# Kernel optimization log

Hardware: AMD Instinct MI355X
Metric: run time of the kernel (lower is better)

Reference implementation:

```python
import jax, jax.numpy as jnp
import numpy as np

B, S, V, E, H, NL, DFF = 16, 16, 64, 64, 8, 4, 2048
L = S * V
DH = E // H
NUM_GRIDS = 100
POI_DIM = 8
OV_DIM = 8


def setup_inputs() -> dict:
    key = jax.random.key(0)
    ks = jax.random.split(key, 32)
    sc = 0.05
    inp = {}
    inp['features'] = jax.random.normal(ks[0], (B, S, V, 3), jnp.float32)
    inp['overlap_tag'] = jax.random.randint(ks[1], (B, S, V), 0, 3)
    inp['poi_id'] = jax.random.randint(ks[2], (B, S, V), 0, NUM_GRIDS + 1)
    # embedders
    inp['W_raw'] = jax.random.normal(ks[3], (3, E), jnp.float32) * sc
    inp['b_raw'] = jnp.zeros((E,), jnp.float32)
    inp['pos_tab'] = jax.random.normal(ks[4], (S, E), jnp.float32) * sc
    inp['type_tab'] = jax.random.normal(ks[5], (V, E), jnp.float32) * sc
    inp['poi_tab'] = jax.random.normal(ks[6], (NUM_GRIDS + 1, POI_DIM), jnp.float32) * sc
    inp['overlap_tab'] = jax.random.normal(ks[7], (3, OV_DIM), jnp.float32) * sc
    inp['W_comb'] = jax.random.normal(ks[8], (E + OV_DIM + POI_DIM, E), jnp.float32) * sc
    inp['b_comb'] = jnp.zeros((E,), jnp.float32)
    # transformer layers (stacked over NL)
    inp['Wqkv'] = jax.random.normal(ks[9], (NL, E, 3 * E), jnp.float32) * sc
    inp['bqkv'] = jnp.zeros((NL, 3 * E), jnp.float32)
    inp['Wo'] = jax.random.normal(ks[10], (NL, E, E), jnp.float32) * sc
    inp['bo'] = jnp.zeros((NL, E), jnp.float32)
    inp['ln1_s'] = jnp.ones((NL, E), jnp.float32)
    inp['ln1_b'] = jnp.zeros((NL, E), jnp.float32)
    inp['W1'] = jax.random.normal(ks[11], (NL, E, DFF), jnp.float32) * sc
    inp['b1'] = jnp.zeros((NL, DFF), jnp.float32)
    inp['W2'] = jax.random.normal(ks[12], (NL, DFF, E), jnp.float32) * sc
    inp['b2'] = jnp.zeros((NL, E), jnp.float32)
    inp['ln2_s'] = jnp.ones((NL, E), jnp.float32)
    inp['ln2_b'] = jnp.zeros((NL, E), jnp.float32)
    inp['W_head'] = jax.random.normal(ks[13], (E, 3), jnp.float32) * sc
    inp['b_head'] = jnp.zeros((3,), jnp.float32)
    return inp


def _layer_norm(x, s, b):
    m = x.mean(-1, keepdims=True)
    v = ((x - m) ** 2).mean(-1, keepdims=True)
    return (x - m) / jnp.sqrt(v + 1e-5) * s + b


def _forward(features, overlap_tag, poi_id, W_raw, b_raw, pos_tab, type_tab,
             poi_tab, overlap_tab, W_comb, b_comb, Wqkv, bqkv, Wo, bo,
             ln1_s, ln1_b, W1, b1, W2, b2, ln2_s, ln2_b, W_head, b_head):
    # padding_idx=0 rows are zero (as in nn.Embedding(padding_idx=0))
    poi_tab = poi_tab.at[0].set(0.0)
    overlap_tab = overlap_tab.at[0].set(0.0)

    zero_mask = (features.sum(-1) == 0).reshape(B, L)  # [B, L]
    ov_idx = jnp.maximum(overlap_tag, 0)
    poi_idx = jnp.maximum(poi_id, 0)

    feat_e = features @ W_raw + b_raw                    # [B,S,V,E]
    concat = jnp.concatenate([feat_e, overlap_tab[ov_idx], poi_tab[poi_idx]], axis=-1)
    x = (concat @ W_comb + b_comb).reshape(B, L, E)      # [B,L,E]

    t_idx = jnp.repeat(jnp.arange(S), V)                 # [L]
    v_idx = jnp.tile(jnp.arange(V), S)                   # [L]
    struct_mask = (t_idx[:, None] != t_idx[None, :]) & (v_idx[:, None] != v_idx[None, :])
    full_mask = struct_mask[None] | zero_mask[:, None, :] | zero_mask[:, :, None]  # [B,L,L]
    bias = jnp.where(full_mask, -jnp.inf, 0.0)[:, None, :, :]  # [B,1,L,L]

    x = x + pos_tab[t_idx][None] + type_tab[v_idx][None]

    scale = 1.0 / jnp.sqrt(jnp.asarray(DH, x.dtype))
    for l in range(NL):
        qkv = x @ Wqkv[l] + bqkv[l]                      # [B,L,3E]
        q, k, v = jnp.split(qkv, 3, axis=-1)
        q = q.reshape(B, L, H, DH)
        k = k.reshape(B, L, H, DH)
        v = v.reshape(B, L, H, DH)
        scores = jnp.einsum('bqhd,bkhd->bhqk', q, k) * scale + bias
        attn = jax.nn.softmax(scores, axis=-1)
        o = jnp.einsum('bhqk,bkhd->bqhd', attn, v).reshape(B, L, E)
        x = _layer_norm(x + o @ Wo[l] + bo[l], ln1_s[l], ln1_b[l])
        ff = jax.nn.relu(x @ W1[l] + b1[l]) @ W2[l] + b2[l]
        x = _layer_norm(x + ff, ln2_s[l], ln2_b[l])

    last = x.reshape(B, S, V, E)[:, -1]                  # [B,V,E]
    return last @ W_head + b_head                        # [B,V,3]


def reference(features, overlap_tag, poi_id, W_raw, b_raw, pos_tab, type_tab,
              poi_tab, overlap_tab, W_comb, b_comb, Wqkv, bqkv, Wo, bo,
              ln1_s, ln1_b, W1, b1, W2, b2, ln2_s, ln2_b, W_head, b_head):
    return _forward(features, overlap_tag, poi_id, W_raw, b_raw, pos_tab, type_tab,
                    poi_tab, overlap_tab, W_comb, b_comb, Wqkv, bqkv, Wo, bo,
                    ln1_s, ln1_b, W1, b1, W2, b2, ln2_s, ln2_b, W_head, b_head)
```

## Files before the change

### kernel.cpp

```cpp
#include <hip/hip_runtime.h>
#include <math.h>

#define BB 16
#define SS 16
#define VVV 64
#define EE 64
#define HHH 8
#define NLAYER 4
#define DFF_ 2048
#define LL 1024
#define BL 16384
#define PERL 131072

typedef __attribute__((ext_vector_type(8))) _Float16 half8;
typedef __attribute__((ext_vector_type(4))) _Float16 half4v;
typedef __attribute__((ext_vector_type(2))) _Float16 half2v;
typedef __attribute__((ext_vector_type(4))) float f32x4;

#if defined(__has_builtin)
#if __has_builtin(__builtin_amdgcn_fdot2)
#define HAVE_FDOT2 1
#endif
#endif

#define SW64(m, k)  (((m) << 6) + ((((k) >> 3) ^ ((m) & 7)) << 3) + ((k) & 7))


__global__ __launch_bounds__(256) void k_prep(
    const float* __restrict__ W1, const float* __restrict__ W2,
    const float* __restrict__ Wqkv, const float* __restrict__ Wo,
    const float* __restrict__ Wcomb,
    _Float16* __restrict__ w1f, _Float16* __restrict__ w2f,
    _Float16* __restrict__ wqkvf, _Float16* __restrict__ wof,
    _Float16* __restrict__ wcombt)
{
  __shared__ float t[64 * 65];
  int bx = blockIdx.x;
  int cc = threadIdx.x & 63, rr = threadIdx.x >> 6;

  if (bx >= 272) {
    int r0 = (bx - 272) * 64;
#pragma unroll
    for (int i = 0; i < 16; i++) {
      int r = i * 4 + rr;
      if (r0 + r < 80) t[r * 65 + cc] = Wcomb[(size_t)(r0 + r) * 64 + cc];
    }
    __syncthreads();
#pragma unroll
    for (int i = 0; i < 16; i++) {
      int c = i * 4 + rr;
      if (r0 + c < 80) wcombt[(size_t)cc * 80 + r0 + c] = (_Float16)t[c * 65 + cc];
    }
    return;
  }

  const float* src; _Float16* dst; int astr;
  if (bx < 128) {
    int l = bx >> 5, g = bx & 31;
    src = W1 + (size_t)l * PERL + g * 64; astr = 2048;
    dst = w1f + (size_t)(l * 32 + g) * 4096;
  } else if (bx < 256) {
    int j = bx - 128; int l = j >> 5, g = j & 31;
    src = W2 + (size_t)l * PERL + (size_t)g * 64 * 64; astr = 64;
    dst = w2f + (size_t)(l * 32 + g) * 4096;
  } else if (bx < 268) {
    int j = bx - 256; int l = j / 3, g = j % 3;
    src = Wqkv + (size_t)l * 64 * 192 + g * 64; astr = 192;
    dst = wqkvf + (size_t)(l * 3 + g) * 4096;
  } else {
    int l = bx - 268;
    src = Wo + (size_t)l * 4096; astr = 64;
    dst = wof + (size_t)l * 4096;
  }
#pragma unroll
  for (int i = 0; i < 16; i++) {
    int a = i * 4 + rr;
    t[cc * 65 + a] = src[(size_t)a * astr + cc];
  }
  __syncthreads();
#pragma unroll
  for (int it = 0; it < 2; it++) {
    int c = threadIdx.x + it * 256;
    int frag = c >> 6, lane = c & 63;
    int m = (frag >> 1) * 16 + (lane & 15);
    int k0 = (frag & 1) * 32 + (lane >> 4) * 8;
    const float* tr = &t[m * 65 + k0];
    half8 h;
#pragma unroll
    for (int j = 0; j < 8; j++) h[j] = (_Float16)tr[j];
    *(half8*)&dst[(size_t)c * 8] = h;
  }
}

__device__ __forceinline__ void qkv_nb(
    const half8 (&af)[2][2], const _Float16* __restrict__ wqkvf,
    const float* __restrict__ bqkv, _Float16* __restrict__ qbuf,
    _Float16* __restrict__ kbuf, _Float16* __restrict__ vbuf,
    int bx, int nb, int wm, int wn, int lane)
{
  int quad = lane >> 4, l15 = lane & 15;
  const _Float16* bt = wqkvf + (size_t)nb * 4096;
  half8 bf[2][2];
#pragma unroll
  for (int nt = 0; nt < 2; nt++)
#pragma unroll
    for (int ks = 0; ks < 2; ks++)
      bf[nt][ks] = *(const half8*)&bt[(size_t)(((wn * 2 + nt) * 2 + ks) * 512) +
                                      lane * 8];
  f32x4 acc[2][2];
#pragma unroll
  for (int mt = 0; mt < 2; mt++)
#pragma unroll
    for (int nt = 0; nt < 2; nt++) {
      float bv = bqkv[nb * 64 + wn * 32 + nt * 16 + l15];
      acc[mt][nt] = (f32x4){bv, bv, bv, bv};
    }
#pragma unroll
  for (int ks = 0; ks < 2; ks++)
#pragma unroll
    for (int mt = 0; mt < 2; mt++)
#pragma unroll
      for (int nt = 0; nt < 2; nt++)
        acc[mt][nt] = __builtin_amdgcn_mfma_f32_16x16x32_f16(
            af[mt][ks], bf[nt][ks], acc[mt][nt], 0, 0, 0);
  _Float16* dst = (nb == 0) ? qbuf : ((nb == 1) ? kbuf : vbuf);
#pragma unroll
  for (int mt = 0; mt < 2; mt++)
#pragma unroll
    for (int nt = 0; nt < 2; nt++) {
      int col = wn * 32 + nt * 16 + l15;
      int h = col >> 3, d = col & 7;
#pragma unroll
      for (int r = 0; r < 4; r++) {
        int row = bx * 64 + wm * 32 + mt * 16 + quad * 4 + r;
        int b = row >> 10, rb = row & 1023;
        dst[((size_t)(b * 8 + h) * 1024 + rb) * 8 + d] = (_Float16)acc[mt][nt][r];
      }
    }
}

__device__ __forceinline__ void ffn_loadw(const _Float16* __restrict__ wt,
                                          half8 (&fr)[4][2], int lane)
{
#pragma unroll
  for (int t = 0; t < 4; t++)
#pragma unroll
    for (int ks = 0; ks < 2; ks++)
      fr[t][ks] = *(const half8*)&wt[(size_t)((t * 2 + ks) * 512) + lane * 8];
}

__device__ __forceinline__ void ffn_chunk(
    const half8 (&a1)[4][2], const half8 (&wb2)[4][2], const half8 (&xb)[2][2],
    _Float16* hw, const float* __restrict__ b1, int g, f32x4 (&acc)[2][4],
    int quad, int l15)
{
  f32x4 hacc[4][2];
#pragma unroll
  for (int ht = 0; ht < 4; ht++)
#pragma unroll
    for (int mt = 0; mt < 2; mt++) hacc[ht][mt] = (f32x4){0.f, 0.f, 0.f, 0.f};
#pragma unroll
  for (int ks = 0; ks < 2; ks++)
#pragma unroll
    for (int ht = 0; ht < 4; ht++)
#pragma unroll
      for (int mt = 0; mt < 2; mt++)
        hacc[ht][mt] = __builtin_amdgcn_mfma_f32_16x16x32_f16(
            a1[ht][ks], xb[mt][ks], hacc[ht][mt], 0, 0, 0);
#pragma unroll
  for (int ht = 0; ht < 4; ht++) {
    float4 bb = *(const float4*)&b1[g * 64 + ht * 16 + quad * 4];
#pragma unroll
    for (int mt = 0; mt < 2; mt++) {
      f32x4 hv = hacc[ht][mt];
      half4v hp = (half4v){
          (_Float16)fmaxf(hv[0] + bb.x, 0.f), (_Float16)fmaxf(hv[1] + bb.y, 0.f),
          (_Float16)fmaxf(hv[2] + bb.z, 0.f), (_Float16)fmaxf(hv[3] + bb.w, 0.f)};
      *(half4v*)&hw[SW64(mt * 16 + l15, ht * 16 + quad * 4)] = hp;
    }
  }
#pragma unroll
  for (int ks = 0; ks < 2; ks++)
#pragma unroll
    for (int mt = 0; mt < 2; mt++) {
      half8 a2 = *(const half8*)&hw[SW64(mt * 16 + l15, ks * 32 + quad * 8)];
#pragma unroll
      for (int nt = 0; nt < 4; nt++)
        acc[mt][nt] = __builtin_amdgcn_mfma_f32_16x16x32_f16(a2, wb2[nt][ks],
                                                             acc[mt][nt], 0, 0, 0);
    }
}

__global__ __launch_bounds__(256) void k_embqkv(
    const float* __restrict__ features, const int* __restrict__ ovtag,
    const int* __restrict__ poiid, const float* __restrict__ W_raw,
    const float* __restrict__ b_raw, const float* __restrict__ ov_tab,
    const float* __restrict__ poi_tab, const _Float16* __restrict__ wcombt,
    const float* __restrict__ b_comb, const float* __restrict__ pos_tab,
    const float* __restrict__ type_tab, float* __restrict__ x1,
    float* __restrict__ zm, const _Float16* __restrict__ wqkvf,
    const float* __restrict__ bqkv, _Float16* __restrict__ qbuf,
    _Float16* __restrict__ kbuf, _Float16* __restrict__ vbuf)
{
  constexpr int KP = 104;
  __shared__ _Float16 As[64 * KP];
  __shared__ _Float16 Bs[64 * KP];
  __shared__ _Float16 xs[4096];
  int tid = threadIdx.x;
  int bx = blockIdx.x;
  int m0 = bx * 64;
  int wave = tid >> 6, lane = tid & 63, quad = lane >> 4, l15 = lane & 15;
  int wm = wave >> 1, wn = wave & 1;
  for (int p = tid; p < 1536; p += 256) {
    int r = p / 24, s = p - r * 24; int c = s * 4;
    int row = m0 + r;
    float f0 = features[row * 3 + 0];
    float f1 = features[row * 3 + 1];
    float f2 = features[row * 3 + 2];
    if (s == 0) zm[row] = ((f0 + f1 + f2) == 0.f) ? 1.f : 0.f;
    half4v h;
#pragma unroll
    for (int j = 0; j < 4; j++) {
      int cc = c + j; float v;
      if (cc < 64) {
        v = b_raw[cc] + f0 * W_raw[cc] + f1 * W_raw[64 + cc] + f2 * W_raw[128 + cc];
      } else if (cc < 72) {
        int tt = ovtag[row]; v = (tt <= 0) ? 0.f : ov_tab[tt * 8 + cc - 64];
      } else if (cc < 80) {
        int tt = poiid[row]; v = (tt <= 0) ? 0.f : poi_tab[tt * 8 + cc - 72];
      } else v = 0.f;
      h[j] = (_Float16)v;
    }
    *(half4v*)&As[r * KP + c] = h;
  }
  for (int p = tid; p < 1536; p += 256) {
    int r = p / 24, s = p - r * 24; int c = s * 4;
    half4v h = (half4v){0, 0, 0, 0};
    if (c < 80) h = *(const half4v*)&wcombt[r * 80 + c];
    *(half4v*)&Bs[r * KP + c] = h;
  }
  __syncthreads();
  f32x4 acc[2][2];
#pragma unroll
  for (int mt = 0; mt < 2; mt++)
#pragma unroll
    for (int nt = 0; nt < 2; nt++) {
      float bv = b_comb[wn * 32 + nt * 16 + l15];
      acc[mt][nt] = (f32x4){bv, bv, bv, bv};
    }
#pragma unroll
  for (int ks = 0; ks < 3; ks++) {
    half8 af[2], bf[2];
#pragma unroll
    for (int mt = 0; mt < 2; mt++)
      af[mt] = *(const half8*)&As[(wm * 32 + mt * 16 + l15) * KP + ks * 32 + quad * 8];
#pragma unroll
    for (int nt = 0; nt < 2; nt++)
      bf[nt] = *(const half8*)&Bs[(wn * 32 + nt * 16 + l15) * KP + ks * 32 + quad * 8];
#pragma unroll
    for (int mt = 0; mt < 2; mt++)
#pragma unroll
      for (int nt = 0; nt < 2; nt++)
        acc[mt][nt] = __builtin_amdgcn_mfma_f32_16x16x32_f16(af[mt], bf[nt],
                                                             acc[mt][nt], 0, 0, 0);
  }
#pragma unroll
  for (int mt = 0; mt < 2; mt++)
#pragma unroll
    for (int nt = 0; nt < 2; nt++)
#pragma unroll
      for (int r = 0; r < 4; r++) {
        int lrow = wm * 32 + mt * 16 + quad * 4 + r;
        int row = m0 + lrow;
        int col = wn * 32 + nt * 16 + l15;
        int l = row & (LL - 1);
        float v = acc[mt][nt][r] +
            pos_tab[(l >> 6) * 64 + col] + type_tab[(l & 63) * 64 + col];
        x1[(size_t)row * 64 + col] = v;
        xs[SW64(lrow, col)] = (_Float16)v;
      }
  __syncthreads();
  half8 af[2][2];
#pragma unroll
  for (int mt = 0; mt < 2; mt++)
#pragma unroll
    for (int ks = 0; ks < 2; ks++)
      af[mt][ks] = *(const half8*)&xs[SW64(wm * 32 + mt * 16 + l15,
                                           ks * 32 + quad * 8)];
  for (int nb = 0; nb < 3; nb++)
    qkv_nb(af, wqkvf, bqkv, qbuf, kbuf, vbuf, bx, nb, wm, wn, lane);
}

__global__ __launch_bounds__(256, 2) void k_layerf(
    const _Float16* __restrict__ qin, const _Float16* __restrict__ kin,
    const _Float16* __restrict__ vin, const float* __restrict__ zm,
    const _Float16* __restrict__ wof, const float* __restrict__ bo,
    float* __restrict__ x1,
    const float* __restrict__ ln1_s, const float* __restrict__ ln1_b,
    const _Float16* __restrict__ w1f, const _Float16* __restrict__ w2f,
    const float* __restrict__ b1, const float* __restrict__ b2,
    const float* __restrict__ ln2_s, const float* __restrict__ ln2_b,
    const _Float16* __restrict__ wqkvf, const float* __restrict__ bqkv,
    _Float16* __restrict__ qout, _Float16* __restrict__ kout,
    _Float16* __restrict__ vout, int doqkv,
    const float* __restrict__ Wh, const float* __restrict__ bh,
    float* __restrict__ out)
{
  __shared__ float ots[32 * 68];
  __shared__ float ots2[32 * 68];
  __shared__ __align__(16) _Float16 xs[2048];
  __shared__ float x2f[2048];
  __shared__ __align__(16) _Float16 hs[4][2048];
  __shared__ __align__(16) _Float16 os[2048];
  __shared__ float zsh[1024];
  int tid = threadIdx.x;
  int bx = blockIdx.x;
  int r0 = bx * 32;
  int wave = tid >> 6, lane = tid & 63;
  int quad = lane >> 4, l15 = lane & 15;
  int grp = wave >> 1, wn = wave & 1;
  int b = r0 >> 10;

  for (int p = tid; p < 1024; p += 256)
    zsh[p] = (zm[b * LL + p] != 0.f) ? -20000.f : 0.f;

  half8 obf[2][2];
#pragma unroll
  for (int nt = 0; nt < 2; nt++)
#pragma unroll
    for (int ks = 0; ks < 2; ks++)
      obf[nt][ks] = *(const half8*)&wof[(size_t)(((wn * 2 + nt) * 2 + ks) * 512) +
                                        lane * 8];
  float x1pre[8];
#pragma unroll
  for (int i = 0; i < 8; i++)
    x1pre[i] = x1[(size_t)(r0 + wave * 8 + i) * 64 + lane];
  float ln1sv = ln1_s[lane], ln1bv = ln1_b[lane];
  float ln2sv = ln2_s[lane], ln2bv = ln2_b[lane];
  float fb2 = b2[lane];
  __syncthreads();

  {
    int lr = tid & 31, hh = tid >> 5;
    int rb = (r0 & 1023) + lr;
    int tq = rb >> 6, vq = rb & 63;
    const _Float16* kb = kin + (size_t)(b * 8 + hh) * 8192;
    const _Float16* vb = vin + (size_t)(b * 8 + hh) * 8192;
    half8 qh = *(const half8*)&qin[(size_t)(b * 8 + hh) * 8192 + (size_t)rb * 8];
    const float scale = 0.3535533905932738f;
    float m = -10000.f, lsum = 0.f;
    float acc[8] = {0.f, 0.f, 0.f, 0.f, 0.f, 0.f, 0.f, 0.f};
    bool zmq = (zsh[rb] < -1.f);

    auto attend = [&](int k) {
      half8 kk = *(const half8*)&kb[(size_t)k * 8];
      half8 vv = *(const half8*)&vb[(size_t)k * 8];
      float s = 0.f;
#ifdef HAVE_FDOT2
#pragma unroll
      for (int j = 0; j < 4; j++) {
        half2v qa = (half2v){qh[2 * j], qh[2 * j + 1]};
        half2v ka = (half2v){kk[2 * j], kk[2 * j + 1]};
        s = __builtin_amdgcn_fdot2(qa, ka, s, false);
      }
#else
#pragma unroll
      for (int j = 0; j < 8; j++) s += (float)qh[j] * (float)kk[j];
#endif
      s = s * scale + zsh[k];
      float nm = fmaxf(m, s);
      float r = __expf(m - nm);
      float p = __expf(s - nm);
      lsum = lsum * r + p;
#pragma unroll
      for (int d = 0; d < 8; d++) acc[d] = acc[d] * r + p * (float)vv[d];
      m = nm;
    };

    if (!zmq) {
      for (int vv2 = 0; vv2 < 64; vv2++) attend(tq * 64 + vv2);
      for (int tt = 0; tt < 16; tt++) {
        if (tt == tq) continue;
        attend(tt * 64 + vq);
      }
    }
    float inv = (lsum > 0.f) ? 1.f / lsum : 0.f;
    half8 o;
#pragma unroll
    for (int d = 0; d < 8; d++) o[d] = (_Float16)(acc[d] * inv);
    *(half8*)&os[SW64(lr, hh * 8)] = o;
  }
  __syncthreads();

  {
    half8 af[2];
#pragma unroll
    for (int ks = 0; ks < 2; ks++)
      af[ks] = *(const half8*)&os[SW64(grp * 16 + l15, ks * 32 + quad * 8)];
    f32x4 acc[2];
#pragma unroll
    for (int nt = 0; nt < 2; nt++) {
      float bv = bo[wn * 32 + nt * 16 + l15];
      acc[nt] = (f32x4){bv, bv, bv, bv};
    }
#pragma unroll
    for (int ks = 0; ks < 2; ks++)
#pragma unroll
      for (int nt = 0; nt < 2; nt++)
        acc[nt] = __builtin_amdgcn_mfma_f32_16x16x32_f16(af[ks], obf[nt][ks],
                                                         acc[nt], 0, 0, 0);
#pragma unroll
    for (int nt = 0; nt < 2; nt++)
#pragma unroll
      for (int r = 0; r < 4; r++)
        ots[(grp * 16 + quad * 4 + r) * 68 + wn * 32 + nt * 16 + l15] = acc[nt][r];
  }
  half8 a1x[4][2], b2x[4][2], a1y[4][2], b2y[4][2];
  ffn_loadw(w1f + (size_t)wave * 4096, a1x, lane);
  ffn_loadw(w2f + (size_t)wave * 4096, b2x, lane);
  __syncthreads();
  for (int i = 0; i < 8; i++) {
    int row = wave * 8 + i;
    float val = ots[row * 68 + lane] + x1pre[i];
    float sum = val;
#pragma unroll
    for (int o = 32; o > 0; o >>= 1) sum += __shfl_xor(sum, o);
    float mean = sum * (1.f / 64.f);
    float d = val - mean;
    float sq = d * d;
#pragma unroll
    for (int o = 32; o > 0; o >>= 1) sq += __shfl_xor(sq, o);
    float xv = d * rsqrtf(sq * (1.f / 64.f) + 1e-5f) * ln1sv + ln1bv;
    x2f[row * 64 + lane] = xv;
    xs[SW64(row, lane)] = (_Float16)xv;
  }
  __syncthreads();

  half8 xb[2][2];
#pragma unroll
  for (int mt = 0; mt < 2; mt++)
#pragma unroll
    for (int ks = 0; ks < 2; ks++)
      xb[mt][ks] = *(const half8*)&xs[SW64(mt * 16 + l15, ks * 32 + quad * 8)];
  f32x4 facc[2][4];
#pragma unroll
  for (int mt = 0; mt < 2; mt++)
#pragma unroll
    for (int nt = 0; nt < 4; nt++) facc[mt][nt] = (f32x4){0.f, 0.f, 0.f, 0.f};
  _Float16* hw = &hs[wave][0];
  for (int ii = 0; ii < 4; ii++) {
    int gy = ii * 8 + 4 + wave;
    ffn_loadw(w1f + (size_t)gy * 4096, a1y, lane);
    ffn_loadw(w2f + (size_t)gy * 4096, b2y, lane);
    ffn_chunk(a1x, b2x, xb, hw, b1, ii * 8 + wave, facc, quad, l15);
    if (ii < 3) {
      ffn_loadw(w1f + (size_t)(gy + 4) * 4096, a1x, lane);
      ffn_loadw(w2f + (size_t)(gy + 4) * 4096, b2x, lane);
    }
    ffn_chunk(a1y, b2y, xb, hw, b1, gy, facc, quad, l15);
  }
  if (wave < 2) {
    float* dst = (wave == 0) ? ots : ots2;
#pragma unroll
    for (int mt = 0; mt < 2; mt++)
#pragma unroll
      for (int nt = 0; nt < 4; nt++)
#pragma unroll
        for (int r = 0; r < 4; r++)
          dst[(mt * 16 + quad * 4 + r) * 68 + nt * 16 + l15] = facc[mt][nt][r];
  }
  __syncthreads();
  if (wave >= 2) {
    float* dst = (wave == 2) ? ots : ots2;
#pragma unroll
    for (int mt = 0; mt < 2; mt++)
#pragma unroll
      for (int nt = 0; nt < 4; nt++)
#pragma unroll
        for (int r = 0; r < 4; r++)
          dst[(mt * 16 + quad * 4 + r) * 68 + nt * 16 + l15] += facc[mt][nt][r];
  }
  __syncthreads();
  for (int i = 0; i < 8; i++) {
    int row = wave * 8 + i;
    size_t off = (size_t)(r0 + row) * 64 + lane;
    float val = ots[row * 68 + lane] + ots2[row * 68 + lane] + fb2 +
                x2f[row * 64 + lane];
    float sum = val;
#pragma unroll
    for (int o = 32; o > 0; o >>= 1) sum += __shfl_xor(sum, o);
    float mean = sum * (1.f / 64.f);
    float d = val - mean;
    float sq = d * d;
#pragma unroll
    for (int o = 32; o > 0; o >>= 1) sq += __shfl_xor(sq, o);
    float xv = d * rsqrtf(sq * (1.f / 64.f) + 1e-5f) * ln2sv + ln2bv;
    x1[off] = xv;
    x2f[row * 64 + lane] = xv;
    xs[SW64(row, lane)] = (_Float16)xv;
  }
  if (!doqkv) {
    __syncthreads();
    if ((bx & 31) >= 30 && tid < 96) {
      int bb2 = bx >> 5;
      int i = tid / 3, j = tid - i * 3;
      int vglob = (bx & 1) * 32 + i;
      float a = bh[j];
      for (int e = 0; e < 64; e++)
        a += x2f[i * 64 + e] * Wh[e * 3 + j];
      out[((size_t)(bb2 * 64 + vglob)) * 3 + j] = a;
    }
    return;
  }
  __syncthreads();
  half8 af[2][2];
#pragma unroll
  for (int mt = 0; mt < 2; mt++)
#pragma unroll
    for (int ks = 0; ks < 2; ks++)
      af[mt][ks] = *(const half8*)&xs[SW64(mt * 16 + l15, ks * 32 + quad * 8)];
  for (int nb = 0; nb < 3; nb++) {
    const _Float16* bt = wqkvf + (size_t)nb * 4096;
    half8 bf[2];
#pragma unroll
    for (int ks = 0; ks < 2; ks++)
      bf[ks] = *(const half8*)&bt[(size_t)((wave * 2 + ks) * 512) + lane * 8];
    f32x4 qacc[2];
#pragma unroll
    for (int mt = 0; mt < 2; mt++) {
      float bv = bqkv[nb * 64 + wave * 16 + l15];
      qacc[mt] = (f32x4){bv, bv, bv, bv};
    }
#pragma unroll
    for (int ks = 0; ks < 2; ks++)
#pragma unroll
      for (int mt = 0; mt < 2; mt++)
        qacc[mt] = __builtin_amdgcn_mfma_f32_16x16x32_f16(af[mt][ks], bf[ks],
                                                          qacc[mt], 0, 0, 0);
    _Float16* dst = (nb == 0) ? qout : ((nb == 1) ? kout : vout);
    int col = wave * 16 + l15;
    int h2 = col >> 3, d2 = col & 7;
#pragma unroll
    for (int mt = 0; mt < 2; mt++)
#pragma unroll
      for (int r = 0; r < 4; r++) {
        int row = r0 + mt * 16 + quad * 4 + r;
        int rbq = row & 1023;
        dst[((size_t)(b * 8 + h2) * 1024 + rbq) * 8 + d2] = (_Float16)qacc[mt][r];
      }
  }
}

extern "C" void kernel_launch(void* const* d_in, const int* in_sizes, int n_in,
                              void* d_out, int out_size, void* d_ws, size_t ws_size,
                              hipStream_t stream) {
  const float* features = (const float*)d_in[0];
  const int*   ovtag    = (const int*)d_in[1];
  const int*   poiid    = (const int*)d_in[2];
  const float* W_raw    = (const float*)d_in[3];
  const float* b_raw    = (const float*)d_in[4];
  const float* pos_tab  = (const float*)d_in[5];
  const float* type_tab = (const float*)d_in[6];
  const float* poi_tab  = (const float*)d_in[7];
  const float* ov_tab   = (const float*)d_in[8];
  const float* W_comb   = (const float*)d_in[9];
  const float* b_comb   = (const float*)d_in[10];
  const float* Wqkv     = (const float*)d_in[11];
  const float* bqkv     = (const float*)d_in[12];
  const float* Wo       = (const float*)d_in[13];
  const float* bo       = (const float*)d_in[14];
  const float* ln1_s    = (const float*)d_in[15];
  const float* ln1_b    = (const float*)d_in[16];
  const float* W1       = (const float*)d_in[17];
  const float* b1       = (const float*)d_in[18];
  const float* W2       = (const float*)d_in[19];
  const float* b2       = (const float*)d_in[20];
  const float* ln2_s    = (const float*)d_in[21];
  const float* ln2_b    = (const float*)d_in[22];
  const float* W_head   = (const float*)d_in[23];
  const float* b_head   = (const float*)d_in[24];
  float* out = (float*)d_out;
  float* ws  = (float*)d_ws;

  float* zm  = ws;
  float* x1  = zm + BL;
  _Float16* qbA = (_Float16*)(x1 + (size_t)BL * 64);
  _Float16* kbA = qbA + (size_t)BL * 64;
  _Float16* vbA = kbA + (size_t)BL * 64;
  _Float16* qbB = vbA + (size_t)BL * 64;
  _Float16* kbB = qbB + (size_t)BL * 64;
  _Float16* vbB = kbB + (size_t)BL * 64;
  _Float16* wcombt = vbB + (size_t)BL * 64;
  _Float16* w1f    = wcombt + 5120;
  _Float16* w2f    = w1f + (size_t)NLAYER * PERL;
  _Float16* wqkvf  = w2f + (size_t)NLAYER * PERL;
  _Float16* wof    = wqkvf + (size_t)NLAYER * 3 * 4096;

  k_prep<<<274, 256, 0, stream>>>(W1, W2, Wqkv, Wo, W_comb,
                                  w1f, w2f, wqkvf, wof, wcombt);
  k_embqkv<<<256, 256, 0, stream>>>(features, ovtag, poiid, W_raw, b_raw,
                                    ov_tab, poi_tab, wcombt, b_comb,
                                    pos_tab, type_tab, x1, zm,
                                    wqkvf, bqkv, qbA, kbA, vbA);
  for (int l = 0; l < NLAYER; l++) {
    const _Float16* qin = (l & 1) ? qbB : qbA;
    const _Float16* kin = (l & 1) ? kbB : kbA;
    const _Float16* vin = (l & 1) ? vbB : vbA;
    _Float16* qout = (l & 1) ? qbA : qbB;
    _Float16* kout = (l & 1) ? kbA : kbB;
    _Float16* vout = (l & 1) ? vbA : vbB;
    int doqkv = (l < NLAYER - 1);
    k_layerf<<<512, 256, 0, stream>>>(
        qin, kin, vin, zm,
        wof + (size_t)l * 4096, bo + l * EE, x1,
        ln1_s + l * EE, ln1_b + l * EE,
        w1f + (size_t)l * PERL, w2f + (size_t)l * PERL,
        b1 + l * DFF_, b2 + l * EE,
        ln2_s + l * EE, ln2_b + l * EE,
        wqkvf + (size_t)(l + 1 < NLAYER ? l + 1 : 0) * 3 * 4096,
        bqkv + (l + 1 < NLAYER ? l + 1 : 0) * 192,
        qout, kout, vout, doqkv, W_head, b_head, out);
  }
}
```

Before: 291.4 us.

## Halve rows per layer block, split attention keys across thread pairs, stage QKV stores

The fused layer kernel now processes 16 rows per block instead of 32 and launches 1024 blocks with a higher occupancy hint. Attention splits each query's key set between two threads and merges their online-softmax state with shuffles. The FFN loop drops the double-buffered weight prefetch, and the next-layer QKV output is staged in shared memory so it can be written with vectorized 16-byte stores. This raises parallelism and occupancy, at the cost of each block re-reading the full FFN weights for half as many rows.

```diff
diff --git a/kernel.cpp b/kernel.cpp
--- a/kernel.cpp
+++ b/kernel.cpp
@@ -136,58 +136,6 @@
         int b = row >> 10, rb = row & 1023;
         dst[((size_t)(b * 8 + h) * 1024 + rb) * 8 + d] = (_Float16)acc[mt][nt][r];
       }
-    }
-}
-
-__device__ __forceinline__ void ffn_loadw(const _Float16* __restrict__ wt,
-                                          half8 (&fr)[4][2], int lane)
-{
-#pragma unroll
-  for (int t = 0; t < 4; t++)
-#pragma unroll
-    for (int ks = 0; ks < 2; ks++)
-      fr[t][ks] = *(const half8*)&wt[(size_t)((t * 2 + ks) * 512) + lane * 8];
-}
-
-__device__ __forceinline__ void ffn_chunk(
-    const half8 (&a1)[4][2], const half8 (&wb2)[4][2], const half8 (&xb)[2][2],
-    _Float16* hw, const float* __restrict__ b1, int g, f32x4 (&acc)[2][4],
-    int quad, int l15)
-{
-  f32x4 hacc[4][2];
-#pragma unroll
-  for (int ht = 0; ht < 4; ht++)
-#pragma unroll
-    for (int mt = 0; mt < 2; mt++) hacc[ht][mt] = (f32x4){0.f, 0.f, 0.f, 0.f};
-#pragma unroll
-  for (int ks = 0; ks < 2; ks++)
-#pragma unroll
-    for (int ht = 0; ht < 4; ht++)
-#pragma unroll
-      for (int mt = 0; mt < 2; mt++)
-        hacc[ht][mt] = __builtin_amdgcn_mfma_f32_16x16x32_f16(
-            a1[ht][ks], xb[mt][ks], hacc[ht][mt], 0, 0, 0);
-#pragma unroll
-  for (int ht = 0; ht < 4; ht++) {
-    float4 bb = *(const float4*)&b1[g * 64 + ht * 16 + quad * 4];
-#pragma unroll
-    for (int mt = 0; mt < 2; mt++) {
-      f32x4 hv = hacc[ht][mt];
-      half4v hp = (half4v){
-          (_Float16)fmaxf(hv[0] + bb.x, 0.f), (_Float16)fmaxf(hv[1] + bb.y, 0.f),
-          (_Float16)fmaxf(hv[2] + bb.z, 0.f), (_Float16)fmaxf(hv[3] + bb.w, 0.f)};
-      *(half4v*)&hw[SW64(mt * 16 + l15, ht * 16 + quad * 4)] = hp;
-    }
-  }
-#pragma unroll
-  for (int ks = 0; ks < 2; ks++)
-#pragma unroll
-    for (int mt = 0; mt < 2; mt++) {
-      half8 a2 = *(const half8*)&hw[SW64(mt * 16 + l15, ks * 32 + quad * 8)];
-#pragma unroll
-      for (int nt = 0; nt < 4; nt++)
-        acc[mt][nt] = __builtin_amdgcn_mfma_f32_16x16x32_f16(a2, wb2[nt][ks],
-                                                             acc[mt][nt], 0, 0, 0);
     }
 }
 
@@ -291,7 +239,7 @@
     qkv_nb(af, wqkvf, bqkv, qbuf, kbuf, vbuf, bx, nb, wm, wn, lane);
 }
 
-__global__ __launch_bounds__(256, 2) void k_layerf(
+__global__ __launch_bounds__(256, 4) void k_layer16(
     const _Float16* __restrict__ qin, const _Float16* __restrict__ kin,
     const _Float16* __restrict__ vin, const float* __restrict__ zm,
     const _Float16* __restrict__ wof, const float* __restrict__ bo,
@@ -306,44 +254,45 @@
     const float* __restrict__ Wh, const float* __restrict__ bh,
     float* __restrict__ out)
 {
-  __shared__ float ots[32 * 68];
-  __shared__ float ots2[32 * 68];
-  __shared__ __align__(16) _Float16 xs[2048];
-  __shared__ float x2f[2048];
-  __shared__ __align__(16) _Float16 hs[4][2048];
-  __shared__ __align__(16) _Float16 os[2048];
+  __shared__ float ots[16 * 68];
+  __shared__ float ots2[16 * 68];
+  __shared__ __align__(16) _Float16 xs[1024];
+  __shared__ float x2f[1024];
+  __shared__ __align__(16) _Float16 hs[4][1024];
+  __shared__ __align__(16) _Float16 os[1024];
   __shared__ float zsh[1024];
+  __shared__ __align__(16) _Float16 qkvt[16 * 200];
   int tid = threadIdx.x;
   int bx = blockIdx.x;
-  int r0 = bx * 32;
+  int r0 = bx * 16;
+  int rb0 = r0 & 1023;
+  int b = r0 >> 10;
   int wave = tid >> 6, lane = tid & 63;
   int quad = lane >> 4, l15 = lane & 15;
-  int grp = wave >> 1, wn = wave & 1;
-  int b = r0 >> 10;
 
   for (int p = tid; p < 1024; p += 256)
     zsh[p] = (zm[b * LL + p] != 0.f) ? -20000.f : 0.f;
 
-  half8 obf[2][2];
-#pragma unroll
-  for (int nt = 0; nt < 2; nt++)
-#pragma unroll
-    for (int ks = 0; ks < 2; ks++)
-      obf[nt][ks] = *(const half8*)&wof[(size_t)(((wn * 2 + nt) * 2 + ks) * 512) +
-                                        lane * 8];
-  float x1pre[8];
-#pragma unroll
-  for (int i = 0; i < 8; i++)
-    x1pre[i] = x1[(size_t)(r0 + wave * 8 + i) * 64 + lane];
+  half8 obf[2];
+#pragma unroll
+  for (int ks = 0; ks < 2; ks++)
+    obf[ks] = *(const half8*)&wof[(size_t)((wave * 2 + ks) * 512) + lane * 8];
+  float x1pre[4];
+#pragma unroll
+  for (int i = 0; i < 4; i++)
+    x1pre[i] = x1[(size_t)(r0 + wave * 4 + i) * 64 + lane];
   float ln1sv = ln1_s[lane], ln1bv = ln1_b[lane];
   float ln2sv = ln2_s[lane], ln2bv = ln2_b[lane];
   float fb2 = b2[lane];
+  float bov = bo[wave * 16 + l15];
   __syncthreads();
 
   {
-    int lr = tid & 31, hh = tid >> 5;
-    int rb = (r0 & 1023) + lr;
-    int tq = rb >> 6, vq = rb & 63;
+    int pr = tid >> 1, ksl = tid & 1;
+    int lr = pr & 15, hh = pr >> 4;
+    int rb = rb0 + lr;
+    int tq = rb0 >> 6;
+    int vq = rb & 63;
     const _Float16* kb = kin + (size_t)(b * 8 + hh) * 8192;
     const _Float16* vb = vin + (size_t)(b * 8 + hh) * 8192;
     half8 qh = *(const half8*)&qin[(size_t)(b * 8 + hh) * 8192 + (size_t)rb * 8];
@@ -378,17 +327,30 @@
     };
 
     if (!zmq) {
-      for (int vv2 = 0; vv2 < 64; vv2++) attend(tq * 64 + vv2);
+      for (int i = 0; i < 32; i++) attend(tq * 64 + 2 * i + ksl);
+      int c = 0;
       for (int tt = 0; tt < 16; tt++) {
         if (tt == tq) continue;
-        attend(tt * 64 + vq);
+        if ((c & 1) == ksl) attend(tt * 64 + vq);
+        c++;
       }
     }
+    float m2 = __shfl_xor(m, 1), l2 = __shfl_xor(lsum, 1);
+    float nm = fmaxf(m, m2);
+    float f1 = __expf(m - nm), f2 = __expf(m2 - nm);
+    lsum = lsum * f1 + l2 * f2;
+#pragma unroll
+    for (int d = 0; d < 8; d++) {
+      float a2 = __shfl_xor(acc[d], 1);
+      acc[d] = acc[d] * f1 + a2 * f2;
+    }
     float inv = (lsum > 0.f) ? 1.f / lsum : 0.f;
-    half8 o;
-#pragma unroll
-    for (int d = 0; d < 8; d++) o[d] = (_Float16)(acc[d] * inv);
-    *(half8*)&os[SW64(lr, hh * 8)] = o;
+    if (ksl == 0) {
+      half8 o;
+#pragma unroll
+      for (int d = 0; d < 8; d++) o[d] = (_Float16)(acc[d] * inv);
+      *(half8*)&os[SW64(lr, hh * 8)] = o;
+    }
   }
   __syncthreads();
 
@@ -396,31 +358,18 @@
     half8 af[2];
 #pragma unroll
     for (int ks = 0; ks < 2; ks++)
-      af[ks] = *(const half8*)&os[SW64(grp * 16 + l15, ks * 32 + quad * 8)];
-    f32x4 acc[2];
-#pragma unroll
-    for (int nt = 0; nt < 2; nt++) {
-      float bv = bo[wn * 32 + nt * 16 + l15];
-      acc[nt] = (f32x4){bv, bv, bv, bv};
-    }
+      af[ks] = *(const half8*)&os[SW64(l15, ks * 32 + quad * 8)];
+    f32x4 acc = (f32x4){bov, bov, bov, bov};
 #pragma unroll
     for (int ks = 0; ks < 2; ks++)
-#pragma unroll
-      for (int nt = 0; nt < 2; nt++)
-        acc[nt] = __builtin_amdgcn_mfma_f32_16x16x32_f16(af[ks], obf[nt][ks],
-                                                         acc[nt], 0, 0, 0);
-#pragma unroll
-    for (int nt = 0; nt < 2; nt++)
-#pragma unroll
-      for (int r = 0; r < 4; r++)
-        ots[(grp * 16 + quad * 4 + r) * 68 + wn * 32 + nt * 16 + l15] = acc[nt][r];
-  }
-  half8 a1x[4][2], b2x[4][2], a1y[4][2], b2y[4][2];
-  ffn_loadw(w1f + (size_t)wave * 4096, a1x, lane);
-  ffn_loadw(w2f + (size_t)wave * 4096, b2x, lane);
-  __syncthreads();
-  for (int i = 0; i < 8; i++) {
-    int row = wave * 8 + i;
+      acc = __builtin_amdgcn_mfma_f32_16x16x32_f16(af[ks], obf[ks], acc, 0, 0, 0);
+#pragma unroll
+    for (int r = 0; r < 4; r++)
+      ots[(quad * 4 + r) * 68 + wave * 16 + l15] = acc[r];
+  }
+  __syncthreads();
+  for (int i = 0; i < 4; i++) {
+    int row = wave * 4 + i;
     float val = ots[row * 68 + lane] + x1pre[i];
     float sum = val;
 #pragma unroll
@@ -436,53 +385,73 @@
   }
   __syncthreads();
 
-  half8 xb[2][2];
-#pragma unroll
-  for (int mt = 0; mt < 2; mt++)
+  half8 xb[2];
+#pragma unroll
+  for (int ks = 0; ks < 2; ks++)
+    xb[ks] = *(const half8*)&xs[SW64(l15, ks * 32 + quad * 8)];
+  f32x4 facc[4];
+#pragma unroll
+  for (int nt = 0; nt < 4; nt++) facc[nt] = (f32x4){0.f, 0.f, 0.f, 0.f};
+  _Float16* hw = &hs[wave][0];
+  for (int ii = 0; ii < 8; ii++) {
+    int g = ii * 4 + wave;
+    const _Float16* w1t = w1f + (size_t)g * 4096;
+    const _Float16* w2t = w2f + (size_t)g * 4096;
+    half8 a1[4][2], b2w[4][2];
+#pragma unroll
+    for (int t = 0; t < 4; t++)
+#pragma unroll
+      for (int ks = 0; ks < 2; ks++) {
+        a1[t][ks] = *(const half8*)&w1t[(size_t)((t * 2 + ks) * 512) + lane * 8];
+        b2w[t][ks] = *(const half8*)&w2t[(size_t)((t * 2 + ks) * 512) + lane * 8];
+      }
+    f32x4 hacc[4];
+#pragma unroll
+    for (int ht = 0; ht < 4; ht++) hacc[ht] = (f32x4){0.f, 0.f, 0.f, 0.f};
 #pragma unroll
     for (int ks = 0; ks < 2; ks++)
-      xb[mt][ks] = *(const half8*)&xs[SW64(mt * 16 + l15, ks * 32 + quad * 8)];
-  f32x4 facc[2][4];
-#pragma unroll
-  for (int mt = 0; mt < 2; mt++)
-#pragma unroll
-    for (int nt = 0; nt < 4; nt++) facc[mt][nt] = (f32x4){0.f, 0.f, 0.f, 0.f};
-  _Float16* hw = &hs[wave][0];
-  for (int ii = 0; ii < 4; ii++) {
-    int gy = ii * 8 + 4 + wave;
-    ffn_loadw(w1f + (size_t)gy * 4096, a1y, lane);
-    ffn_loadw(w2f + (size_t)gy * 4096, b2y, lane);
-    ffn_chunk(a1x, b2x, xb, hw, b1, ii * 8 + wave, facc, quad, l15);
-    if (ii < 3) {
-      ffn_loadw(w1f + (size_t)(gy + 4) * 4096, a1x, lane);
-      ffn_loadw(w2f + (size_t)(gy + 4) * 4096, b2x, lane);
-    }
-    ffn_chunk(a1y, b2y, xb, hw, b1, gy, facc, quad, l15);
+#pragma unroll
+      for (int ht = 0; ht < 4; ht++)
+        hacc[ht] = __builtin_amdgcn_mfma_f32_16x16x32_f16(a1[ht][ks], xb[ks],
+                                                          hacc[ht], 0, 0, 0);
+#pragma unroll
+    for (int ht = 0; ht < 4; ht++) {
+      float4 bb = *(const float4*)&b1[g * 64 + ht * 16 + quad * 4];
+      f32x4 hv = hacc[ht];
+      half4v hp = (half4v){
+          (_Float16)fmaxf(hv[0] + bb.x, 0.f), (_Float16)fmaxf(hv[1] + bb.y, 0.f),
+          (_Float16)fmaxf(hv[2] + bb.z, 0.f), (_Float16)fmaxf(hv[3] + bb.w, 0.f)};
+      *(half4v*)&hw[SW64(l15, ht * 16 + quad * 4)] = hp;
+    }
+#pragma unroll
+    for (int ks = 0; ks < 2; ks++) {
+      half8 a2 = *(const half8*)&hw[SW64(l15, ks * 32 + quad * 8)];
+#pragma unroll
+      for (int nt = 0; nt < 4; nt++)
+        facc[nt] = __builtin_amdgcn_mfma_f32_16x16x32_f16(a2, b2w[nt][ks],
+                                                          facc[nt], 0, 0, 0);
+    }
   }
   if (wave < 2) {
     float* dst = (wave == 0) ? ots : ots2;
 #pragma unroll
-    for (int mt = 0; mt < 2; mt++)
-#pragma unroll
-      for (int nt = 0; nt < 4; nt++)
-#pragma unroll
-        for (int r = 0; r < 4; r++)
-          dst[(mt * 16 + quad * 4 + r) * 68 + nt * 16 + l15] = facc[mt][nt][r];
+    for (int nt = 0; nt < 4; nt++)
+#pragma unroll
+      for (int r = 0; r < 4; r++)
+        dst[(quad * 4 + r) * 68 + nt * 16 + l15] = facc[nt][r];
   }
   __syncthreads();
   if (wave >= 2) {
     float* dst = (wave == 2) ? ots : ots2;
 #pragma unroll
-    for (int mt = 0; mt < 2; mt++)
-#pragma unroll
-      for (int nt = 0; nt < 4; nt++)
-#pragma unroll
-        for (int r = 0; r < 4; r++)
-          dst[(mt * 16 + quad * 4 + r) * 68 + nt * 16 + l15] += facc[mt][nt][r];
-  }
-  __syncthreads();
-  for (int i = 0; i < 8; i++) {
-    int row = wave * 8 + i;
+    for (int nt = 0; nt < 4; nt++)
+#pragma unroll
+      for (int r = 0; r < 4; r++)
+        dst[(quad * 4 + r) * 68 + nt * 16 + l15] += facc[nt][r];
+  }
+  __syncthreads();
+  for (int i = 0; i < 4; i++) {
+    int row = wave * 4 + i;
     size_t off = (size_t)(r0 + row) * 64 + lane;
     float val = ots[row * 68 + lane] + ots2[row * 68 + lane] + fb2 +
                 x2f[row * 64 + lane];
@@ -499,12 +468,12 @@
     x2f[row * 64 + lane] = xv;
     xs[SW64(row, lane)] = (_Float16)xv;
   }
+  __syncthreads();
   if (!doqkv) {
-    __syncthreads();
-    if ((bx & 31) >= 30 && tid < 96) {
-      int bb2 = bx >> 5;
+    if ((bx & 63) >= 60 && tid < 48) {
+      int bb2 = bx >> 6;
       int i = tid / 3, j = tid - i * 3;
-      int vglob = (bx & 1) * 32 + i;
+      int vglob = (bx & 3) * 16 + i;
       float a = bh[j];
       for (int e = 0; e < 64; e++)
         a += x2f[i * 64 + e] * Wh[e * 3 + j];
@@ -512,42 +481,37 @@
     }
     return;
   }
-  __syncthreads();
-  half8 af[2][2];
-#pragma unroll
-  for (int mt = 0; mt < 2; mt++)
+  {
+    half8 af[2];
 #pragma unroll
     for (int ks = 0; ks < 2; ks++)
-      af[mt][ks] = *(const half8*)&xs[SW64(mt * 16 + l15, ks * 32 + quad * 8)];
-  for (int nb = 0; nb < 3; nb++) {
-    const _Float16* bt = wqkvf + (size_t)nb * 4096;
-    half8 bf[2];
-#pragma unroll
-    for (int ks = 0; ks < 2; ks++)
-      bf[ks] = *(const half8*)&bt[(size_t)((wave * 2 + ks) * 512) + lane * 8];
-    f32x4 qacc[2];
-#pragma unroll
-    for (int mt = 0; mt < 2; mt++) {
+      af[ks] = *(const half8*)&xs[SW64(l15, ks * 32 + quad * 8)];
+#pragma unroll
+    for (int nb = 0; nb < 3; nb++) {
+      const _Float16* bt = wqkvf + (size_t)nb * 4096;
+      half8 bf[2];
+#pragma unroll
+      for (int ks = 0; ks < 2; ks++)
+        bf[ks] = *(const half8*)&bt[(size_t)((wave * 2 + ks) * 512) + lane * 8];
       float bv = bqkv[nb * 64 + wave * 16 + l15];
-      qacc[mt] = (f32x4){bv, bv, bv, bv};
-    }
-#pragma unroll
-    for (int ks = 0; ks < 2; ks++)
-#pragma unroll
-      for (int mt = 0; mt < 2; mt++)
-        qacc[mt] = __builtin_amdgcn_mfma_f32_16x16x32_f16(af[mt][ks], bf[ks],
-                                                          qacc[mt], 0, 0, 0);
-    _Float16* dst = (nb == 0) ? qout : ((nb == 1) ? kout : vout);
-    int col = wave * 16 + l15;
-    int h2 = col >> 3, d2 = col & 7;
-#pragma unroll
-    for (int mt = 0; mt < 2; mt++)
-#pragma unroll
-      for (int r = 0; r < 4; r++) {
-        int row = r0 + mt * 16 + quad * 4 + r;
-        int rbq = row & 1023;
-        dst[((size_t)(b * 8 + h2) * 1024 + rbq) * 8 + d2] = (_Float16)qacc[mt][r];
-      }
+      f32x4 qacc = (f32x4){bv, bv, bv, bv};
+#pragma unroll
+      for (int ks = 0; ks < 2; ks++)
+        qacc = __builtin_amdgcn_mfma_f32_16x16x32_f16(af[ks], bf[ks], qacc,
+                                                      0, 0, 0);
+#pragma unroll
+      for (int r = 0; r < 4; r++)
+        qkvt[(quad * 4 + r) * 200 + nb * 64 + wave * 16 + l15] = (_Float16)qacc[r];
+    }
+  }
+  __syncthreads();
+  for (int p = tid; p < 384; p += 256) {
+    int buf = p >> 7;
+    int idx = p & 127;
+    int h = idx >> 4, lr = idx & 15;
+    _Float16* dst = (buf == 0) ? qout : ((buf == 1) ? kout : vout);
+    half8 v = *(const half8*)&qkvt[lr * 200 + buf * 64 + h * 8];
+    *(half8*)&dst[((size_t)(b * 8 + h) * 1024 + rb0 + lr) * 8] = v;
   }
 }
 
@@ -610,7 +574,7 @@
     _Float16* kout = (l & 1) ? kbA : kbB;
     _Float16* vout = (l & 1) ? vbA : vbB;
     int doqkv = (l < NLAYER - 1);
-    k_layerf<<<512, 256, 0, stream>>>(
+    k_layer16<<<1024, 256, 0, stream>>>(
         qin, kin, vin, zm,
         wof + (size_t)l * 4096, bo + l * EE, x1,
         ln1_s + l * EE, ln1_b + l * EE,
```

Result: slower. 318.0 us (+9.2%).
